# Optimization experiments

Hardware: AMD Instinct MI355X
Metric: run time of the kernel (lower is better)

The kernel has to match this reference:

```python
import jax, jax.numpy as jnp
import numpy as np

NUM_FRAMES = 24
FRAME_SIZE = 8          # heads per frame; attention_probs.shape[0] = NUM_FRAMES*FRAME_SIZE
DIM_X = 32
DIM_Y = 32
SEQ = 300
STRENGTHEN_SCALE = 0.125
WEAKEN_SCALE = 0.918
INJECTION_SCALE = 1.0
KERNEL_DIVISION = 3.0
LEN_PROMPT = 8          # 'A basketball player missing a three-point shot'
TRAILING = 100
# token_inds=[2,3] union trailing range (9..108); order irrelevant (uniform write)
TOKEN_INDS = np.array(sorted(set([2, 3]) | set(range(LEN_PROMPT + 1, LEN_PROMPT + TRAILING + 1))), dtype=np.int32)
_LEFTS = [0.05, 0.0717, 0.0935, 0.1152, 0.137, 0.1587, 0.1804, 0.2022, 0.2239, 0.2457,
          0.2674, 0.2891, 0.3109, 0.3326, 0.3543, 0.3761, 0.3978, 0.4196, 0.4413, 0.463,
          0.4848, 0.5065, 0.5283, 0.55]
# [top, left, bottom, right] ratios per frame (matches init_kwargs bbox_per_frame)
BBOX_PER_FRAME = [(0.25, l, 0.75, round(l + 0.3, 4)) for l in _LEFTS]


def _bbox_px(ratios, dim_x, dim_y):
    top = int(dim_y * ratios[0]); left = int(dim_x * ratios[1])
    bottom = int(dim_y * ratios[2]); right = int(dim_x * ratios[3])
    return top, left, bottom, right


def _gauss_patch(h, w):
    # torch.linspace(0, h, h): h points, endpoint inclusive; mx=int(h/2), sx=h/3
    x = jnp.linspace(0.0, float(h), h)[:, None]
    y = jnp.linspace(0.0, float(w), w)[None, :]
    sx, sy = h / KERNEL_DIVISION, w / KERNEL_DIVISION
    g = jnp.exp(-(((x - h // 2) ** 2) / (2.0 * sx * sx) + ((y - w // 2) ** 2) / (2.0 * sy * sy)))
    return g / g.max()  # 1/(2*pi*sx*sy) prefactor cancels under max-normalization


def _forward(attention_probs, dim_x, dim_y):
    F = NUM_FRAMES
    fs = attention_probs.shape[0] // F
    seq = attention_probs.shape[-1]
    max_val = attention_probs.max()
    scale = max_val * INJECTION_SCALE
    # strengthen map is identical across heads-within-frame and across selected tokens:
    # build a compact [F, dim_y, dim_x] map instead of the full 4D zeros_like tensor.
    wm = jnp.zeros((F, dim_y, dim_x), attention_probs.dtype)
    for i, r in enumerate(BBOX_PER_FRAME):  # fixed small frame count, trace-time loop
        t, l, b, rt = _bbox_px(r, dim_x, dim_y)
        wm = wm.at[i, t:b, l:rt].set(_gauss_patch(b - t, rt - l).astype(attention_probs.dtype) * scale)
    inds = TOKEN_INDS
    ap5 = attention_probs.reshape(F, fs, dim_y, dim_x, seq)
    sel = ap5[..., inds]                     # [F, fs, dy, dx, T]
    wmb = wm[:, None, :, :, None]            # broadcast over heads & tokens
    weaken = jnp.where(wmb == 0, WEAKEN_SCALE, 1.0).astype(attention_probs.dtype)
    new_sel = sel * weaken + STRENGTHEN_SCALE * wmb
    out = ap5.at[..., inds].set(new_sel)
    return out.reshape(attention_probs.shape)


def setup_inputs() -> dict:
    key = jax.random.key(0)
    ap = jax.random.uniform(key, (NUM_FRAMES * FRAME_SIZE, DIM_Y, DIM_X, SEQ), dtype=jnp.float32)
    return {"attention_probs": ap, "dim_x": DIM_X, "dim_y": DIM_Y}


def reference(attention_probs, dim_x, dim_y):
    return _forward(attention_probs, dim_x, dim_y)
```

## Files before the change

### kernel.cpp

```cpp
#include <hip/hip_runtime.h>

#define SEQ        300
#define V4         (SEQ / 4)
#define NROWS      (192 * 32 * 32)
#define N4         (NROWS * V4)
#define NFRAMES    24
#define P1BLOCKS   (N4 / 256)

__constant__ int c_left[NFRAMES]  = {1,2,2,3,4,5,5,6,7,7,8,9,9,10,11,12,12,13,14,14,15,16,16,17};
__constant__ int c_width[NFRAMES] = {10,9,10,10,9,9,10,10,9,10,10,9,10,10,9,9,10,10,9,10,10,9,10,10};

__device__ __forceinline__ float wave_max64(float v) {
    #pragma unroll
    for (int off = 32; off > 0; off >>= 1)
        v = fmaxf(v, __shfl_down(v, off, 64));
    return v;
}

__global__ void kphase1(const float4* __restrict__ in, float4* __restrict__ out,
                        float* __restrict__ bmax) {
    int idx = blockIdx.x * 256 + threadIdx.x;
    int row = idx / V4;
    int c   = idx - row * V4;
    int f   = row >> 13;
    int yy  = (row >> 5) & 31;
    int xx  = row & 31;
    int l   = c_left[f];
    bool inB = (yy >= 8) & (yy < 24) & (xx >= l) & (xx < l + c_width[f]);

    float4 v = in[idx];
    float m = fmaxf(fmaxf(v.x, v.y), fmaxf(v.z, v.w));

    float r[4] = {v.x, v.y, v.z, v.w};
    if (!inB) {
        int s0 = c * 4;
        #pragma unroll
        for (int k = 0; k < 4; k++) {
            int s = s0 + k;
            bool tok = (s == 2) | (s == 3) | ((s >= 9) & (s <= 108));
            if (tok) r[k] *= 0.918f;
        }
    }
    out[idx] = make_float4(r[0], r[1], r[2], r[3]);

    m = wave_max64(m);
    __shared__ float sw[4];
    int lane = threadIdx.x & 63, wv = threadIdx.x >> 6;
    if (lane == 0) sw[wv] = m;
    __syncthreads();
    if (threadIdx.x == 0)
        bmax[blockIdx.x] = fmaxf(fmaxf(sw[0], sw[1]), fmaxf(sw[2], sw[3]));
}

__global__ void kwm(const float* __restrict__ bmax, float* __restrict__ wm) {
    __shared__ float patch[16 * 10];
    __shared__ float sw[4];
    __shared__ float s_scale, s_gmax;
    const int f = blockIdx.x;
    const int tid = threadIdx.x;

    float m = 0.0f;
    for (int i = tid; i < P1BLOCKS; i += 256) m = fmaxf(m, bmax[i]);
    m = wave_max64(m);
    if ((tid & 63) == 0) sw[tid >> 6] = m;
    __syncthreads();
    if (tid == 0) s_scale = fmaxf(fmaxf(sw[0], sw[1]), fmaxf(sw[2], sw[3]));

    const int w = c_width[f], l = c_left[f];
    if (tid < 16 * w) {
        int i = tid / w, j = tid - i * w;
        float x = (float)i * (16.0f / 15.0f);
        float y = (float)j * ((float)w / (float)(w - 1));
        float dx = x - 8.0f;
        float dy = y - (float)(w / 2);
        float sx = 16.0f / 3.0f;
        float sy = (float)w / 3.0f;
        patch[tid] = expf(-(dx * dx / (2.0f * sx * sx) + dy * dy / (2.0f * sy * sy)));
    }
    __syncthreads();
    if (tid == 0) {
        float g = 0.0f;
        for (int k = 0; k < 16 * w; k++) g = fmaxf(g, patch[k]);
        s_gmax = g;
    }
    __syncthreads();
    const float mul = s_scale / s_gmax;
    for (int p = tid; p < 1024; p += 256) {
        int yy = p >> 5, xx = p & 31;
        float v = 0.0f;
        if (yy >= 8 && yy < 24 && xx >= l && xx < l + w)
            v = patch[(yy - 8) * w + (xx - l)] * mul;
        wm[f * 1024 + p] = v;
    }
}

__global__ void kinject(float* __restrict__ out, const float* __restrict__ wm) {
    const int b  = blockIdx.x;
    const int f  = b >> 7;
    const int fs = (b >> 4) & 7;
    const int yy = (b & 15) + 8;
    const int l  = c_left[f], w = c_width[f];
    const int r0 = ((f * 8 + fs) * 32 + yy) * 32;
    const int total = w * 102;

    for (int t = threadIdx.x; t < total; t += 256) {
        int xi = t / 102;
        int si = t - xi * 102;
        int s  = (si < 2) ? (si + 2) : (si + 7);
        float add = 0.125f * wm[f * 1024 + yy * 32 + l + xi];
        out[(r0 + l + xi) * SEQ + s] += add;
    }
}

extern "C" void kernel_launch(void* const* d_in, const int* in_sizes, int n_in,
                              void* d_out, int out_size, void* d_ws, size_t ws_size,
                              hipStream_t stream) {
    const float* ap = (const float*)d_in[0];
    float* out = (float*)d_out;
    float* ws  = (float*)d_ws;
    float* bmax = ws;
    float* wm   = ws + P1BLOCKS;

    kphase1<<<P1BLOCKS, 256, 0, stream>>>((const float4*)ap, (float4*)out, bmax);
    kwm<<<NFRAMES, 256, 0, stream>>>(bmax, wm);
    kinject<<<24 * 8 * 16, 256, 0, stream>>>(out, wm);
}
```

Before: 426.8 us.

## Unroll phase-1 streaming 4x with nontemporal loads/stores and constant weight table

Each thread in the streaming pass now handles four float4 elements strided by a quarter of the tensor, issuing all loads before any compute so more memory requests are in flight. Loads and stores use nontemporal builtins to avoid polluting the cache, and the per-token weaken factor comes from a 300-entry constant table instead of per-element branching. This cuts the block count by four and the number of bmax partials kwm has to reduce. The cost is higher register use per thread and reliance on the stride mapping being exactly aligned to frame boundaries (FSTEP).

```diff
diff --git a/kernel.cpp b/kernel.cpp
--- a/kernel.cpp
+++ b/kernel.cpp
@@ -5,10 +5,32 @@
 #define NROWS      (192 * 32 * 32)
 #define N4         (NROWS * V4)
 #define NFRAMES    24
-#define P1BLOCKS   (N4 / 256)
+#define UNROLL     4
+#define TTOT       (N4 / UNROLL)
+#define P1BLOCKS   (TTOT / 256)
+#define ROWSTEP    (TTOT / V4)
+#define FSTEP      (ROWSTEP >> 13)
+
+typedef float f32x4 __attribute__((ext_vector_type(4)));
 
 __constant__ int c_left[NFRAMES]  = {1,2,2,3,4,5,5,6,7,7,8,9,9,10,11,12,12,13,14,14,15,16,16,17};
 __constant__ int c_width[NFRAMES] = {10,9,10,10,9,9,10,10,9,10,10,9,10,10,9,9,10,10,9,10,10,9,10,10};
+
+#define Wq 0.918f
+#define W4 Wq,Wq,Wq,Wq,
+#define O4 1.0f,1.0f,1.0f,1.0f,
+__constant__ __align__(16) float c_wf[300] = {
+    1.0f,1.0f,Wq,Wq,
+    O4
+    1.0f,Wq,Wq,Wq,
+    W4 W4 W4 W4 W4 W4 W4 W4 W4 W4 W4 W4
+    W4 W4 W4 W4 W4 W4 W4 W4 W4 W4 W4 W4
+    Wq,1.0f,1.0f,1.0f,
+    O4 O4 O4 O4 O4 O4 O4 O4 O4 O4 O4 O4
+    O4 O4 O4 O4 O4 O4 O4 O4 O4 O4 O4 O4
+    O4 O4 O4 O4 O4 O4 O4 O4 O4 O4 O4 O4
+    O4 O4 O4 O4 O4 O4 O4 O4 O4 O4 O4
+};
 
 __device__ __forceinline__ float wave_max64(float v) {
     #pragma unroll
@@ -17,35 +39,38 @@
     return v;
 }
 
-__global__ void kphase1(const float4* __restrict__ in, float4* __restrict__ out,
-                        float* __restrict__ bmax) {
-    int idx = blockIdx.x * 256 + threadIdx.x;
-    int row = idx / V4;
-    int c   = idx - row * V4;
-    int f   = row >> 13;
-    int yy  = (row >> 5) & 31;
-    int xx  = row & 31;
-    int l   = c_left[f];
-    bool inB = (yy >= 8) & (yy < 24) & (xx >= l) & (xx < l + c_width[f]);
+__global__ void __launch_bounds__(256) kphase1(const f32x4* __restrict__ in,
+                                               f32x4* __restrict__ out,
+                                               float* __restrict__ bmax) {
+    const int t    = blockIdx.x * 256 + threadIdx.x;
+    const int row0 = t / V4;
+    const int c    = t - row0 * V4;
+    const int f0   = row0 >> 13;
+    const int yy   = (row0 >> 5) & 31;
+    const int xx   = row0 & 31;
+    const bool yIn = (yy >= 8) & (yy < 24);
+    const f32x4 wf = ((const f32x4*)c_wf)[c];
 
-    float4 v = in[idx];
-    float m = fmaxf(fmaxf(v.x, v.y), fmaxf(v.z, v.w));
+    f32x4 v[UNROLL];
+    #pragma unroll
+    for (int j = 0; j < UNROLL; j++)
+        v[j] = __builtin_nontemporal_load(in + t + j * TTOT);
 
-    float r[4] = {v.x, v.y, v.z, v.w};
-    if (!inB) {
-        int s0 = c * 4;
-        #pragma unroll
-        for (int k = 0; k < 4; k++) {
-            int s = s0 + k;
-            bool tok = (s == 2) | (s == 3) | ((s >= 9) & (s <= 108));
-            if (tok) r[k] *= 0.918f;
-        }
+    float m = 0.0f;
+    #pragma unroll
+    for (int j = 0; j < UNROLL; j++) {
+        f32x4 x = v[j];
+        m = fmaxf(m, fmaxf(fmaxf(x[0], x[1]), fmaxf(x[2], x[3])));
+        const int f = f0 + j * FSTEP;
+        const int l = c_left[f];
+        const bool inB = yIn & (xx >= l) & (xx < l + c_width[f]);
+        f32x4 r = inB ? x : (x * wf);
+        __builtin_nontemporal_store(r, out + t + j * TTOT);
     }
-    out[idx] = make_float4(r[0], r[1], r[2], r[3]);
 
     m = wave_max64(m);
     __shared__ float sw[4];
-    int lane = threadIdx.x & 63, wv = threadIdx.x >> 6;
+    const int lane = threadIdx.x & 63, wv = threadIdx.x >> 6;
     if (lane == 0) sw[wv] = m;
     __syncthreads();
     if (threadIdx.x == 0)
@@ -121,7 +146,7 @@
     float* bmax = ws;
     float* wm   = ws + P1BLOCKS;
 
-    kphase1<<<P1BLOCKS, 256, 0, stream>>>((const float4*)ap, (float4*)out, bmax);
+    kphase1<<<P1BLOCKS, 256, 0, stream>>>((const f32x4*)ap, (f32x4*)out, bmax);
     kwm<<<NFRAMES, 256, 0, stream>>>(bmax, wm);
     kinject<<<24 * 8 * 16, 256, 0, stream>>>(out, wm);
 }
```

Result: faster. 404.9 us (-5.1%).
